# Kernel tuning notes

Hardware: AMD Instinct MI355X
Metric: run time of the kernel (lower is better)

The kernel has to match this reference:

```python
import jax, jax.numpy as jnp
import numpy as np

K = 3       # attractive nearest neighbors
J = 3       # repulsive offset (uses dist[:, :, J:])
ALPHA = 0.1
NU = 1e-3


def setup_inputs() -> dict:
    key = jax.random.key(0)
    k1, k2 = jax.random.split(key, 2)
    phi_p = jax.random.normal(k1, (4, 512, 64, 64), dtype=jnp.float32)
    memory_bank = jax.random.normal(k2, (16384, 512), dtype=jnp.float32)
    r = jnp.ones((1,), dtype=jnp.float32)
    return {"phi_p": phi_p, "memory_bank": memory_bank, "r": r}


def reference(phi_p, memory_bank, r):
    B, C, H, W = phi_p.shape
    # b c h w -> b (h w) c
    x = phi_p.reshape(B, C, H * W).transpose(0, 2, 1)
    x2 = jnp.sum(x * x, axis=-1, keepdims=True)            # [B, HW, 1]
    m2 = jnp.sum(memory_bank * memory_bank, axis=-1)       # [N]
    d2 = x2 + m2[None, None, :] - 2.0 * jnp.einsum('bnc,mc->bnm', x, memory_bank)
    d2 = jnp.maximum(d2, 0.0)                              # [B, HW, N]
    # smallest K+J squared distances, ascending (topk(largest=False))
    neg_top, _ = jax.lax.top_k(-d2, K + J)
    dist = -neg_top                                        # [B, HW, K+J]
    r2 = r ** 2
    scores_att = dist[:, :, :K] - r2
    loss_att = jnp.mean(jnp.maximum(scores_att, 0.0)) / NU
    scores_rep = r2 - dist[:, :, J:] - ALPHA
    loss_rep = jnp.mean(jnp.maximum(scores_rep, 0.0)) / NU
    return loss_att + loss_rep
```

## Files before the change

### kernel.cpp

```cpp
#include <hip/hip_runtime.h>
#include <cfloat>

#define B_   4
#define C_   512
#define HW_  4096
#define R_   16384
#define N_   16384
#define ALPHA_ 0.1f
#define SCALE_ ((float)(1000.0/49152.0))

#define NCHUNK 4

typedef unsigned int u32;
typedef unsigned short u16;
typedef unsigned char u8;
typedef __attribute__((ext_vector_type(2))) unsigned long long u64x2;
typedef __attribute__((ext_vector_type(4))) float f32x4;

typedef const __attribute__((address_space(1))) u32* gas_u32;
typedef __attribute__((address_space(3))) u32* las_u32;

__device__ __forceinline__ void async16(const void* g, void* l) {
    __builtin_amdgcn_global_load_lds((gas_u32)g, (las_u32)l, 16, 0, 0);
}

__device__ __forceinline__ u32 pk_fp8x4(float a, float b, float c, float d) {
    u32 v = __builtin_amdgcn_cvt_pk_fp8_f32(a, b, 0, false);
    v = __builtin_amdgcn_cvt_pk_fp8_f32(c, d, v, true);
    return v;
}

__device__ __forceinline__ void ins6(float (&t)[6], float v) {
    if (v < t[5]) {
        t[5] = v;
        #pragma unroll
        for (int q = 5; q >= 1; --q) {
            float lo = fminf(t[q-1], t[q]);
            float hi = fmaxf(t[q-1], t[q]);
            t[q-1] = lo; t[q] = hi;
        }
    }
}

__global__ void conv_mem_kernel(const float* __restrict__ mem,
                                u8* __restrict__ Mb, float* __restrict__ m2) {
    int w = threadIdx.x >> 6, l = threadIdx.x & 63;
    int row = blockIdx.x * 4 + w;
    const float4* p = (const float4*)(mem + (size_t)row * C_);
    float4 a = p[l], b = p[l + 64];
    float s = a.x*a.x + a.y*a.y + a.z*a.z + a.w*a.w
            + b.x*b.x + b.y*b.y + b.z*b.z + b.w*b.w;
    *(u32*)(Mb + (size_t)row * C_ + l*4)       = pk_fp8x4(a.x, a.y, a.z, a.w);
    *(u32*)(Mb + (size_t)row * C_ + 256 + l*4) = pk_fp8x4(b.x, b.y, b.z, b.w);
    #pragma unroll
    for (int off = 32; off > 0; off >>= 1) s += __shfl_down(s, off);
    if (l == 0) m2[row] = s;
}

__global__ void conv_phi_kernel(const float* __restrict__ phi, u8* __restrict__ Xb,
                                float* __restrict__ x2) {
    __shared__ float T[64][65];
    int t = threadIdx.x;
    int n0 = blockIdx.x * 64, c0 = blockIdx.y * 64, b = blockIdx.z;
    const float* src = phi + ((size_t)b * C_ + c0) * HW_ + n0;
    int l = t & 63, cg = t >> 6;
    float sq = 0.f;
    #pragma unroll
    for (int p = 0; p < 16; ++p) {
        int c = cg + p * 4;
        float v = src[(size_t)c * HW_ + l];
        T[c][l] = v;
        sq = fmaf(v, v, sq);
    }
    atomicAdd(&x2[(size_t)b * HW_ + n0 + l], sq);
    __syncthreads();
    int cq = t & 15, gl0 = t >> 4;
    #pragma unroll
    for (int p = 0; p < 4; ++p) {
        int gl = gl0 + p * 16;
        u32 v = pk_fp8x4(T[cq*4+0][gl], T[cq*4+1][gl],
                         T[cq*4+2][gl], T[cq*4+3][gl]);
        size_t g = (size_t)b * HW_ + n0 + gl;
        *(u32*)(Xb + g * C_ + c0 + cq*4) = v;
    }
}

__global__ __launch_bounds__(256, 2) void gemm_topk_kernel(
    const u8* __restrict__ Xb, const u8* __restrict__ Mb,
    const float* __restrict__ m2, float* __restrict__ P ) {
    __shared__ __align__(16) u8 smem[32768];
    u8* Xs = smem;
    u8* Ms = smem + 16384;

    const int t = threadIdx.x;
    const int w = t >> 6, l = t & 63;
    const int g0  = blockIdx.x * 128;
    const int n0c = blockIdx.y * (N_ / NCHUNK);
    const int rh  = w * 32;
    const int fm  = l & 15;
    const int rq  = l >> 4;
    const int pc  = (rq ^ ((fm >> 1) & 3)) * 16;
    const int srow4 = l >> 2;
    const int soff  = (((l & 3) ^ ((l >> 3) & 3)) * 16);

    float top[8][6];
    #pragma unroll
    for (int s8 = 0; s8 < 8; ++s8)
        #pragma unroll
        for (int q = 0; q < 6; ++q) top[s8][q] = FLT_MAX;

    const u8* Xsrc = Xb + (size_t)(g0 + rh) * C_;
    u8* XsW = Xs + rh * 64;
    u8* MsW = Ms + rh * 64;

    for (int nt = 0; nt < N_ / NCHUNK / 128; ++nt) {
        const int n0 = n0c + nt * 128;
        const u8* Msrc = Mb + (size_t)(n0 + rh) * C_;

        float m2w[8];
        #pragma unroll
        for (int n = 0; n < 8; ++n) m2w[n] = m2[n0 + n * 16 + fm];

        f32x4 acc[2][8];
        #pragma unroll
        for (int m = 0; m < 2; ++m)
            #pragma unroll
            for (int n = 0; n < 8; ++n) acc[m][n] = (f32x4)0.f;

        for (int s = 0; s < 4; ++s) {
            const int k0 = s * 128;
            #pragma unroll
            for (int h = 0; h < 2; ++h)
                #pragma unroll
                for (int i = 0; i < 2; ++i) {
                    async16(Xsrc + (size_t)(i*16 + srow4) * C_ + k0 + h*64 + soff,
                            XsW + h*8192 + i*1024);
                    async16(Msrc + (size_t)(i*16 + srow4) * C_ + k0 + h*64 + soff,
                            MsW + h*8192 + i*1024);
                }
            __syncthreads();
            #pragma unroll
            for (int h = 0; h < 2; ++h) {
                const u8* Xh = Xs + h * 8192;
                const u8* Mh = Ms + h * 8192;
                u64x2 av[2], bv[8];
                #pragma unroll
                for (int m = 0; m < 2; ++m)
                    av[m] = *(const u64x2*)(Xh + (rh + m*16 + fm) * 64 + pc);
                #pragma unroll
                for (int n = 0; n < 8; ++n)
                    bv[n] = *(const u64x2*)(Mh + (n*16 + fm) * 64 + pc);
                #pragma unroll
                for (int m = 0; m < 2; ++m)
                    #pragma unroll
                    for (int n = 0; n < 8; ++n)
                        acc[m][n] = __builtin_amdgcn_mfma_f32_16x16x32_fp8_fp8(
                            (long)av[m].x, (long)bv[n].x, acc[m][n], 0, 0, 0);
                #pragma unroll
                for (int m = 0; m < 2; ++m)
                    #pragma unroll
                    for (int n = 0; n < 8; ++n)
                        acc[m][n] = __builtin_amdgcn_mfma_f32_16x16x32_fp8_fp8(
                            (long)av[m].y, (long)bv[n].y, acc[m][n], 0, 0, 0);
            }
            __syncthreads();
        }

        #pragma unroll
        for (int m = 0; m < 2; ++m)
            #pragma unroll
            for (int j = 0; j < 4; ++j) {
                float d0 = m2w[0] - 2.f * acc[m][0][j];
                float d1 = m2w[1] - 2.f * acc[m][1][j];
                float d2 = m2w[2] - 2.f * acc[m][2][j];
                float d3 = m2w[3] - 2.f * acc[m][3][j];
                float d4 = m2w[4] - 2.f * acc[m][4][j];
                float d5 = m2w[5] - 2.f * acc[m][5][j];
                float d6 = m2w[6] - 2.f * acc[m][6][j];
                float d7 = m2w[7] - 2.f * acc[m][7][j];
                float vmin = fminf(fminf(fminf(d0, d1), fminf(d2, d3)),
                                   fminf(fminf(d4, d5), fminf(d6, d7)));
                float (&tt)[6] = top[m * 4 + j];
                if (vmin < tt[5]) {
                    ins6(tt, d0); ins6(tt, d1); ins6(tt, d2); ins6(tt, d3);
                    ins6(tt, d4); ins6(tt, d5); ins6(tt, d6); ins6(tt, d7);
                }
            }
    }

    float* Mg = (float*)smem;
    #pragma unroll 1
    for (int p = 0; p < 2; ++p) {
        __syncthreads();
        if ((w >> 1) == p) {
            #pragma unroll
            for (int m = 0; m < 2; ++m)
                #pragma unroll
                for (int j = 0; j < 4; ++j) {
                    int lrow = (w & 1) * 32 + m * 16 + rq * 4 + j;
                    #pragma unroll
                    for (int q = 0; q < 6; ++q)
                        Mg[lrow * 97 + fm * 6 + q] = top[m * 4 + j][q];
                }
        }
        __syncthreads();
        if (t < 64) {
            float t6[6];
            #pragma unroll
            for (int q = 0; q < 6; ++q) t6[q] = FLT_MAX;
            const float* row = Mg + t * 97;
            for (int v = 0; v < 96; ++v) ins6(t6, row[v]);
            float* dst = P + ((size_t)(g0 + p * 64 + t) * NCHUNK + blockIdx.y) * 6;
            #pragma unroll
            for (int q = 0; q < 6; ++q) dst[q] = t6[q];
        }
    }
}

__global__ void finalize_kernel(const float* __restrict__ P, const float* __restrict__ x2,
                                const float* __restrict__ rp, float* __restrict__ out) {
    int g = blockIdx.x * 256 + threadIdx.x;
    float t6[6];
    #pragma unroll
    for (int q = 0; q < 6; ++q) t6[q] = FLT_MAX;
    const f32x4* pp = (const f32x4*)(P + (size_t)g * (NCHUNK * 6));
    #pragma unroll
    for (int q = 0; q < NCHUNK * 6 / 4; ++q) {
        f32x4 v = pp[q];
        ins6(t6, v.x); ins6(t6, v.y); ins6(t6, v.z); ins6(t6, v.w);
    }
    float x2g = x2[g];
    float rv = rp[0], r2 = rv * rv;
    float s = 0.f;
    #pragma unroll
    for (int i = 0; i < 3; ++i) {
        float d = fmaxf(t6[i] + x2g, 0.f);
        s += fmaxf(d - r2, 0.f);
    }
    #pragma unroll
    for (int i = 3; i < 6; ++i) {
        float d = fmaxf(t6[i] + x2g, 0.f);
        s += fmaxf(r2 - d - ALPHA_, 0.f);
    }
    #pragma unroll
    for (int off = 32; off > 0; off >>= 1) s += __shfl_down(s, off);
    __shared__ float red[4];
    int w = threadIdx.x >> 6, l = threadIdx.x & 63;
    if (l == 0) red[w] = s;
    __syncthreads();
    if (threadIdx.x == 0)
        atomicAdd(out, (red[0] + red[1] + red[2] + red[3]) * SCALE_);
}

#define TM 64
#define TN 64
#define KC 64
#define LDP 68

__global__ void m2_kernel(const float* __restrict__ mem, float* __restrict__ m2) {
    int wave = threadIdx.x >> 6, lane = threadIdx.x & 63;
    int row = blockIdx.x * 4 + wave;
    const float4* p = reinterpret_cast<const float4*>(mem + (size_t)row * C_);
    float4 a = p[lane], b = p[lane + 64];
    float s = a.x*a.x + a.y*a.y + a.z*a.z + a.w*a.w
            + b.x*b.x + b.y*b.y + b.z*b.z + b.w*b.w;
    #pragma unroll
    for (int off = 32; off > 0; off >>= 1) s += __shfl_down(s, off);
    if (lane == 0) m2[row] = s;
}

__global__ void x2f_kernel(const float* __restrict__ phi, float* __restrict__ x2) {
    int g = blockIdx.x * blockDim.x + threadIdx.x;
    int b = g >> 12;
    int n = g & 4095;
    const float* p = phi + (size_t)b * C_ * HW_ + n;
    float s = 0.f;
    #pragma unroll 8
    for (int c = 0; c < C_; ++c) {
        float v = p[(size_t)c * HW_];
        s = fmaf(v, v, s);
    }
    x2[g] = s;
}

__global__ __launch_bounds__(256) void dist_loss_kernel(
    const float* __restrict__ phi, const float* __restrict__ mem,
    const float* __restrict__ rp,  const float* __restrict__ m2,
    const float* __restrict__ x2,  float* __restrict__ out) {
    __shared__ float smem[2 * TM * LDP];
    float* xs = smem;
    float* ms = smem + TM * LDP;
    const int tid = threadIdx.x;
    const int tx = tid & 15, ty = tid >> 4;
    const int g0 = blockIdx.x * TM;
    const int b = g0 >> 12, n0img = g0 & 4095;
    const float* phiB = phi + (size_t)b * C_ * HW_ + n0img;
    float top[4][6];
    #pragma unroll
    for (int i = 0; i < 4; ++i)
        #pragma unroll
        for (int q = 0; q < 6; ++q) top[i][q] = FLT_MAX;
    float x2v[4];
    #pragma unroll
    for (int i = 0; i < 4; ++i) x2v[i] = x2[g0 + ty * 4 + i];
    for (int nt = 0; nt < N_ / TN; ++nt) {
        const int n0 = nt * TN;
        float acc[4][4];
        #pragma unroll
        for (int i = 0; i < 4; ++i)
            #pragma unroll
            for (int j = 0; j < 4; ++j) acc[i][j] = 0.f;
        for (int s = 0; s < C_ / KC; ++s) {
            const int k0 = s * KC;
            {
                int rr = tid & 63, cb = tid >> 6;
                #pragma unroll
                for (int p = 0; p < 16; ++p) {
                    int cc = p * 4 + cb;
                    xs[rr * LDP + cc] = phiB[(size_t)(k0 + cc) * HW_ + rr];
                }
            }
            {
                int kq = tid & 15, cb = tid >> 4;
                #pragma unroll
                for (int p = 0; p < 4; ++p) {
                    int c = p * 16 + cb;
                    float4 v = *reinterpret_cast<const float4*>(
                        mem + (size_t)(n0 + c) * C_ + k0 + kq * 4);
                    ms[(kq*4+0)*LDP + c] = v.x; ms[(kq*4+1)*LDP + c] = v.y;
                    ms[(kq*4+2)*LDP + c] = v.z; ms[(kq*4+3)*LDP + c] = v.w;
                }
            }
            __syncthreads();
            #pragma unroll
            for (int kq = 0; kq < KC / 4; ++kq) {
                float4 xa[4], mb[4];
                #pragma unroll
                for (int i = 0; i < 4; ++i)
                    xa[i] = *reinterpret_cast<const float4*>(&xs[(ty*4+i)*LDP + kq*4]);
                #pragma unroll
                for (int kk = 0; kk < 4; ++kk)
                    mb[kk] = *reinterpret_cast<const float4*>(&ms[(kq*4+kk)*LDP + tx*4]);
                #pragma unroll
                for (int i = 0; i < 4; ++i) {
                    const float xk[4] = {xa[i].x, xa[i].y, xa[i].z, xa[i].w};
                    #pragma unroll
                    for (int kk = 0; kk < 4; ++kk) {
                        const float mc[4] = {mb[kk].x, mb[kk].y, mb[kk].z, mb[kk].w};
                        #pragma unroll
                        for (int j = 0; j < 4; ++j)
                            acc[i][j] = fmaf(xk[kk], mc[j], acc[i][j]);
                    }
                }
            }
            __syncthreads();
        }
        #pragma unroll
        for (int j = 0; j < 4; ++j) {
            float m2v = m2[n0 + tx * 4 + j];
            #pragma unroll
            for (int i = 0; i < 4; ++i) {
                float d = fmaxf(x2v[i] + m2v - 2.f * acc[i][j], 0.f);
                ins6(top[i], d);
            }
        }
    }
    __syncthreads();
    float* mg = smem;
    #pragma unroll
    for (int i = 0; i < 4; ++i)
        #pragma unroll
        for (int q = 0; q < 6; ++q)
            mg[(ty*4+i)*97 + tx*6 + q] = top[i][q];
    __syncthreads();
    if (tid < 64) {
        float t6[6];
        #pragma unroll
        for (int q = 0; q < 6; ++q) t6[q] = FLT_MAX;
        const float* row = mg + tid * 97;
        for (int v = 0; v < 96; ++v) ins6(t6, row[v]);
        float rv = rp[0], r2 = rv * rv;
        float s = fmaxf(t6[0]-r2,0.f) + fmaxf(t6[1]-r2,0.f) + fmaxf(t6[2]-r2,0.f)
                + fmaxf(r2-t6[3]-ALPHA_,0.f) + fmaxf(r2-t6[4]-ALPHA_,0.f)
                + fmaxf(r2-t6[5]-ALPHA_,0.f);
        #pragma unroll
        for (int off = 32; off > 0; off >>= 1) s += __shfl_down(s, off);
        if (tid == 0) atomicAdd(out, s * SCALE_);
    }
}

extern "C" void kernel_launch(void* const* d_in, const int* in_sizes, int n_in,
                              void* d_out, int out_size, void* d_ws, size_t ws_size,
                              hipStream_t stream) {
    const float* phi = (const float*)d_in[0];
    const float* mem = (const float*)d_in[1];
    const float* rp  = (const float*)d_in[2];
    float* out = (float*)d_out;

    const size_t offX  = 0;
    const size_t offM  = (size_t)R_ * C_;
    const size_t offx2 = offM + (size_t)N_ * C_;
    const size_t offm2 = offx2 + (size_t)R_ * 4;
    const size_t offP  = offm2 + (size_t)N_ * 4;
    const size_t need  = offP + (size_t)R_ * NCHUNK * 6 * 4;

    hipMemsetAsync(out, 0, sizeof(float), stream);

    if (ws_size >= need) {
        u8*    Xb = (u8*)((char*)d_ws + offX);
        u8*    Mb = (u8*)((char*)d_ws + offM);
        float* x2 = (float*)((char*)d_ws + offx2);
        float* m2 = (float*)((char*)d_ws + offm2);
        float* P  = (float*)((char*)d_ws + offP);

        hipMemsetAsync(x2, 0, (size_t)R_ * 4, stream);
        conv_mem_kernel<<<N_ / 4, 256, 0, stream>>>(mem, Mb, m2);
        conv_phi_kernel<<<dim3(HW_ / 64, C_ / 64, B_), 256, 0, stream>>>(phi, Xb, x2);
        gemm_topk_kernel<<<dim3(128, NCHUNK), 256, 0, stream>>>(Xb, Mb, m2, P);
        finalize_kernel<<<R_ / 256, 256, 0, stream>>>(P, x2, rp, out);
    } else {
        float* m2 = (float*)d_ws;
        float* x2 = m2 + N_;
        m2_kernel<<<N_ / 4, 256, 0, stream>>>(mem, m2);
        x2f_kernel<<<R_ / 256, 256, 0, stream>>>(phi, x2);
        dist_loss_kernel<<<R_ / TM, 256, 0, stream>>>(phi, mem, rp, m2, x2, out);
    }
}
```

Baseline: 384.3 us.

## Keep X fragments in registers and double-buffer memory-bank tiles in LDS

The per-wave X row fragments for the whole K dimension are loaded once into registers, so X no longer streams through LDS on every N tile. The freed LDS is used as a double buffer for memory-bank tiles. The next K-slice is prefetched asynchronously while MFMAs run on the current one, removing one barrier per step. This costs 16 extra u64x2 registers per thread under launch_bounds(256,2), which may cause spills or lower occupancy. The wait on the prefetched data now relies on a single __syncthreads per step.

```diff
diff --git a/kernel.cpp b/kernel.cpp
--- a/kernel.cpp
+++ b/kernel.cpp
@@ -89,9 +89,6 @@
     const u8* __restrict__ Xb, const u8* __restrict__ Mb,
     const float* __restrict__ m2, float* __restrict__ P ) {
     __shared__ __align__(16) u8 smem[32768];
-    u8* Xs = smem;
-    u8* Ms = smem + 16384;
-
     const int t = threadIdx.x;
     const int w = t >> 6, l = t & 63;
     const int g0  = blockIdx.x * 128;
@@ -103,19 +100,38 @@
     const int srow4 = l >> 2;
     const int soff  = (((l & 3) ^ ((l >> 3) & 3)) * 16);
 
+    u64x2 av[2][4][2];
+    #pragma unroll
+    for (int m = 0; m < 2; ++m) {
+        const u8* Xr = Xb + (size_t)(g0 + rh + m*16 + fm) * C_ + rq * 16;
+        #pragma unroll
+        for (int s = 0; s < 4; ++s)
+            #pragma unroll
+            for (int h = 0; h < 2; ++h)
+                av[m][s][h] = *(const u64x2*)(Xr + s*128 + h*64);
+    }
+
     float top[8][6];
     #pragma unroll
     for (int s8 = 0; s8 < 8; ++s8)
         #pragma unroll
         for (int q = 0; q < 6; ++q) top[s8][q] = FLT_MAX;
 
-    const u8* Xsrc = Xb + (size_t)(g0 + rh) * C_;
-    u8* XsW = Xs + rh * 64;
-    u8* MsW = Ms + rh * 64;
-
-    for (int nt = 0; nt < N_ / NCHUNK / 128; ++nt) {
+    {
+        const u8* Msrc = Mb + (size_t)(n0c + rh) * C_;
+        #pragma unroll
+        for (int h = 0; h < 2; ++h)
+            #pragma unroll
+            for (int i = 0; i < 2; ++i)
+                async16(Msrc + (size_t)(i*16 + srow4) * C_ + h*64 + soff,
+                        smem + rh*64 + h*8192 + i*1024);
+    }
+    __syncthreads();
+
+    const int NT = N_ / NCHUNK / 128;
+    #pragma unroll 1
+    for (int nt = 0; nt < NT; ++nt) {
         const int n0 = n0c + nt * 128;
-        const u8* Msrc = Mb + (size_t)(n0 + rh) * C_;
 
         float m2w[8];
         #pragma unroll
@@ -127,26 +143,27 @@
             #pragma unroll
             for (int n = 0; n < 8; ++n) acc[m][n] = (f32x4)0.f;
 
+        #pragma unroll
         for (int s = 0; s < 4; ++s) {
-            const int k0 = s * 128;
-            #pragma unroll
-            for (int h = 0; h < 2; ++h)
-                #pragma unroll
-                for (int i = 0; i < 2; ++i) {
-                    async16(Xsrc + (size_t)(i*16 + srow4) * C_ + k0 + h*64 + soff,
-                            XsW + h*8192 + i*1024);
-                    async16(Msrc + (size_t)(i*16 + srow4) * C_ + k0 + h*64 + soff,
-                            MsW + h*8192 + i*1024);
+            {
+                const int nt2 = (s == 3) ? nt + 1 : nt;
+                const int s2  = (s + 1) & 3;
+                if (nt2 < NT) {
+                    const u8* Msrc = Mb + (size_t)(n0c + nt2*128 + rh) * C_ + s2*128;
+                    u8* dst = smem + ((s+1)&1)*16384 + rh*64;
+                    #pragma unroll
+                    for (int h = 0; h < 2; ++h)
+                        #pragma unroll
+                        for (int i = 0; i < 2; ++i)
+                            async16(Msrc + (size_t)(i*16 + srow4) * C_ + h*64 + soff,
+                                    dst + h*8192 + i*1024);
                 }
-            __syncthreads();
+            }
+            const u8* bufp = smem + (s&1)*16384;
             #pragma unroll
             for (int h = 0; h < 2; ++h) {
-                const u8* Xh = Xs + h * 8192;
-                const u8* Mh = Ms + h * 8192;
-                u64x2 av[2], bv[8];
-                #pragma unroll
-                for (int m = 0; m < 2; ++m)
-                    av[m] = *(const u64x2*)(Xh + (rh + m*16 + fm) * 64 + pc);
+                const u8* Mh = bufp + h * 8192;
+                u64x2 bv[8];
                 #pragma unroll
                 for (int n = 0; n < 8; ++n)
                     bv[n] = *(const u64x2*)(Mh + (n*16 + fm) * 64 + pc);
@@ -155,37 +172,39 @@
                     #pragma unroll
                     for (int n = 0; n < 8; ++n)
                         acc[m][n] = __builtin_amdgcn_mfma_f32_16x16x32_fp8_fp8(
-                            (long)av[m].x, (long)bv[n].x, acc[m][n], 0, 0, 0);
+                            (long)av[m][s][h].x, (long)bv[n].x, acc[m][n], 0, 0, 0);
                 #pragma unroll
                 for (int m = 0; m < 2; ++m)
                     #pragma unroll
                     for (int n = 0; n < 8; ++n)
                         acc[m][n] = __builtin_amdgcn_mfma_f32_16x16x32_fp8_fp8(
-                            (long)av[m].y, (long)bv[n].y, acc[m][n], 0, 0, 0);
+                            (long)av[m][s][h].y, (long)bv[n].y, acc[m][n], 0, 0, 0);
+            }
+
+            if (s == 3) {
+                #pragma unroll
+                for (int m = 0; m < 2; ++m)
+                    #pragma unroll
+                    for (int j = 0; j < 4; ++j) {
+                        float d0 = m2w[0] - 2.f * acc[m][0][j];
+                        float d1 = m2w[1] - 2.f * acc[m][1][j];
+                        float d2 = m2w[2] - 2.f * acc[m][2][j];
+                        float d3 = m2w[3] - 2.f * acc[m][3][j];
+                        float d4 = m2w[4] - 2.f * acc[m][4][j];
+                        float d5 = m2w[5] - 2.f * acc[m][5][j];
+                        float d6 = m2w[6] - 2.f * acc[m][6][j];
+                        float d7 = m2w[7] - 2.f * acc[m][7][j];
+                        float vmin = fminf(fminf(fminf(d0, d1), fminf(d2, d3)),
+                                           fminf(fminf(d4, d5), fminf(d6, d7)));
+                        float (&tt)[6] = top[m * 4 + j];
+                        if (vmin < tt[5]) {
+                            ins6(tt, d0); ins6(tt, d1); ins6(tt, d2); ins6(tt, d3);
+                            ins6(tt, d4); ins6(tt, d5); ins6(tt, d6); ins6(tt, d7);
+                        }
+                    }
             }
             __syncthreads();
         }
-
-        #pragma unroll
-        for (int m = 0; m < 2; ++m)
-            #pragma unroll
-            for (int j = 0; j < 4; ++j) {
-                float d0 = m2w[0] - 2.f * acc[m][0][j];
-                float d1 = m2w[1] - 2.f * acc[m][1][j];
-                float d2 = m2w[2] - 2.f * acc[m][2][j];
-                float d3 = m2w[3] - 2.f * acc[m][3][j];
-                float d4 = m2w[4] - 2.f * acc[m][4][j];
-                float d5 = m2w[5] - 2.f * acc[m][5][j];
-                float d6 = m2w[6] - 2.f * acc[m][6][j];
-                float d7 = m2w[7] - 2.f * acc[m][7][j];
-                float vmin = fminf(fminf(fminf(d0, d1), fminf(d2, d3)),
-                                   fminf(fminf(d4, d5), fminf(d6, d7)));
-                float (&tt)[6] = top[m * 4 + j];
-                if (vmin < tt[5]) {
-                    ins6(tt, d0); ins6(tt, d1); ins6(tt, d2); ins6(tt, d3);
-                    ins6(tt, d4); ins6(tt, d5); ins6(tt, d6); ins6(tt, d7);
-                }
-            }
     }
 
     float* Mg = (float*)smem;
```

Measured after the change: 385.6 us. About the same (+0.3%).
